# Performance work log

Hardware: AMD Instinct MI355X
Metric: run time of the kernel (lower is better)

Reference implementation:

```python
import math
import jax, jax.numpy as jnp
from jax import lax
import numpy as np

STRIDES = (4, 8, 16, 32, 64)
SIZES = (32, 64, 128, 256, 512)        # one anchor size per level
ASPECTS = (0.5, 1.0, 2.0)              # A = 3 anchors per location
GRIDS = ((336, 512), (168, 256), (84, 128), (42, 64), (21, 32))
OFFSET = 0.0
IMG_H, IMG_W = 1344, 2048
PRE_NMS_TOPK = 1000
POST_NMS_TOPK = 300
NMS_THRESH = 0.7
MIN_SIDE = 0.0
SCALE_CLAMP = math.log(1000.0 / 16.0)  # Box2BoxTransform default
NEG = -1e9                             # finite stand-in for removed/suppressed scores


def _cell_anchors(size):
    # AnchorGenerator.generate_cell_anchors
    area = float(size) ** 2
    out = []
    for ar in ASPECTS:
        w = math.sqrt(area / ar)
        h = ar * w
        out.append([-w / 2.0, -h / 2.0, w / 2.0, h / 2.0])
    return np.asarray(out, np.float32)  # [A,4]


def _level_anchors(level):
    # grid_anchors: shifts (x,y,x,y) + cell anchors, row-major over (y,x)
    gh, gw = GRIDS[level]
    s = float(STRIDES[level])
    sx = (np.arange(gw, dtype=np.float32) + OFFSET) * s
    sy = (np.arange(gh, dtype=np.float32) + OFFSET) * s
    yy, xx = np.meshgrid(sy, sx, indexing='ij')
    shifts = np.stack([xx.ravel(), yy.ravel(), xx.ravel(), yy.ravel()], axis=1)  # [H*W,4]
    cells = _cell_anchors(SIZES[level])  # [A,4]
    return jnp.asarray((shifts[:, None, :] + cells[None, :, :]).reshape(-1, 4))  # [H*W*A,4]


def _apply_deltas(deltas, anchors):
    # Box2BoxTransform.apply_deltas with unit weights. deltas/anchors: [N,K,4]
    w = anchors[..., 2] - anchors[..., 0]
    h = anchors[..., 3] - anchors[..., 1]
    cx = anchors[..., 0] + 0.5 * w
    cy = anchors[..., 1] + 0.5 * h
    dx, dy, dw, dh = (deltas[..., i] for i in range(4))
    pw = jnp.exp(jnp.minimum(dw, SCALE_CLAMP)) * w
    ph = jnp.exp(jnp.minimum(dh, SCALE_CLAMP)) * h
    pcx = dx * w + cx
    pcy = dy * h + cy
    return jnp.stack([pcx - 0.5 * pw, pcy - 0.5 * ph, pcx + 0.5 * pw, pcy + 0.5 * ph], axis=-1)


def _nms(boxes, scores, lvl):
    # batched NMS for one image: offset boxes per level so levels never suppress
    # each other, then iteratively pick argmax and suppress IoU > thresh.
    off = lvl * (float(max(IMG_H, IMG_W)) + 1.0)
    b = boxes + off[:, None]                               # [M,4]
    areas = (b[:, 2] - b[:, 0]) * (b[:, 3] - b[:, 1])

    def step(sc, _):
        i = jnp.argmax(sc)
        best = sc[i]
        lt = jnp.maximum(b[:, :2], b[i, :2])
        rb = jnp.minimum(b[:, 2:], b[i, 2:])
        wh = jnp.clip(rb - lt, 0.0)
        inter = wh[:, 0] * wh[:, 1]
        iou = inter / (areas + areas[i] - inter + 1e-9)
        sc = jnp.where(iou > NMS_THRESH, NEG, sc).at[i].set(NEG)
        return sc, (i, best > NEG * 0.5)

    _, (idx, valid) = lax.scan(step, scores, None, length=POST_NMS_TOPK)
    return idx, valid


def _forward(logits, deltas):
    # per-level sort (top-k) + gather, as in find_top_rpn_proposals
    all_scores, all_boxes, all_lvl = [], [], []
    for lv in range(5):
        sc, idx = lax.top_k(logits[lv], PRE_NMS_TOPK)                       # [N,K]
        d = jnp.take_along_axis(deltas[lv], idx[..., None], axis=1)          # [N,K,4]
        a = _level_anchors(lv)[idx]                                          # [N,K,4]
        all_boxes.append(_apply_deltas(d, a))
        all_scores.append(sc)
        all_lvl.append(jnp.full((PRE_NMS_TOPK,), float(lv), jnp.float32))
    scores = jnp.concatenate(all_scores, axis=1)   # [N, 5K]
    boxes = jnp.concatenate(all_boxes, axis=1)     # [N, 5K, 4]
    lvl = jnp.concatenate(all_lvl, axis=0)         # [5K]

    # _clip_box
    x0 = jnp.clip(boxes[..., 0], 0.0, float(IMG_W))
    y0 = jnp.clip(boxes[..., 1], 0.0, float(IMG_H))
    x1 = jnp.clip(boxes[..., 2], 0.0, float(IMG_W))
    y1 = jnp.clip(boxes[..., 3], 0.0, float(IMG_H))
    boxes = jnp.stack([x0, y0, x1, y1], axis=-1)

    # _nonempty_boxes: mask out instead of dynamic filter
    keep = ((x1 - x0) > MIN_SIDE) & ((y1 - y0) > MIN_SIDE)
    scores = jnp.where(keep, scores, NEG)

    idx, valid = jax.vmap(lambda b, s: _nms(b, s, lvl))(boxes, scores)       # [N,POST]
    ob = jnp.take_along_axis(boxes, idx[..., None], axis=1)                  # [N,POST,4]
    os = jnp.take_along_axis(scores, idx, axis=1)                            # [N,POST]
    ob = jnp.where(valid[..., None], ob, 0.0)
    os = jnp.where(valid, os, NEG)
    return jnp.concatenate([ob, os[..., None]], axis=-1)                     # [N,POST,5]


def setup_inputs() -> dict:
    key = jax.random.key(0)
    N = 8
    counts = [gh * gw * 3 for gh, gw in GRIDS]
    ks = jax.random.split(key, 10)
    inp = {}
    for lv, m in enumerate(counts):
        inp[f'logits{lv}'] = jax.random.normal(ks[2 * lv], (N, m), jnp.float32)
        inp[f'deltas{lv}'] = jax.random.normal(ks[2 * lv + 1], (N, m, 4), jnp.float32)
    return inp


def reference(logits0, deltas0, logits1, deltas1, logits2, deltas2,
              logits3, deltas3, logits4, deltas4):
    logits = [logits0, logits1, logits2, logits3, logits4]
    deltas = [deltas0, deltas1, deltas2, deltas3, deltas4]
    return _forward(logits, deltas)
```

## Files before the change

kernel.cpp:

```cpp
#include <hip/hip_runtime.h>
#include <cstdint>
#include <cstddef>

#define NB1      16384
#define L1SHIFT  18
#define K_TOP    1000
#define NCAND    5000
#define NIMG     8
#define NLVL     5
#define NTASK    40
#define NPOST    300
#define NEGF     (-1e9f)
#define NWORDS   79
#define NPAD     (NWORDS * 64)
#define NSLOT    23
#define SCAP     2048

typedef unsigned long long u64;

struct Ptrs {
    const float* lg[5];
    const float* dl[5];
};

__device__ __forceinline__ unsigned key_of(float f) {
    unsigned u = __float_as_uint(f);
    return (u & 0x80000000u) ? ~u : (u | 0x80000000u);
}

__device__ __forceinline__ void lvl_of_slot(int bx, int& lvl, int& lb, int& gx, int& m) {
    lvl = (bx < 16) ? 0 : (bx < 20) ? 1 : (bx < 21) ? 2 : (bx < 22) ? 3 : 4;
    const int S0[5] = {0, 16, 20, 21, 22};
    const int GX[5] = {16, 4, 1, 1, 1};
    const int MS[5] = {516096, 129024, 32256, 8064, 2016};
    lb = bx - S0[lvl];
    gx = GX[lvl];
    m  = MS[lvl];
}

__global__ __launch_bounds__(1024) void kStage(Ptrs p,
                                               u64* __restrict__ compS,
                                               unsigned* __restrict__ bcnt) {
    int lvl, lb, gx, m;
    lvl_of_slot(blockIdx.x, lvl, lb, gx, m);
    int img = blockIdx.y;
    size_t slice = (size_t)img * NSLOT + blockIdx.x;
    const float* lg = p.lg[lvl];
    const float TF5[5] = {2.75f, 2.3f, 1.7f, 0.9f, -0.35f};
    float Tf = TF5[lvl];
    __shared__ unsigned lcnt;
    int tid = threadIdx.x, lane = tid & 63;
    if (tid == 0) lcnt = 0u;
    __syncthreads();
    int m4 = m >> 2;
    int chunk4 = (m4 + gx - 1) / gx;
    int start4 = lb * chunk4;
    int end4   = min(start4 + chunk4, m4);
    const float4* src = (const float4*)(lg + (size_t)img * m);
    u64 below = (1ULL << lane) - 1ULL;
    for (int ib = start4; ib < end4; ib += 1024) {
        int i = ib + tid;
        bool inb = (i < end4);
        float4 v = inb ? src[i] : make_float4(0.f, 0.f, 0.f, 0.f);
        int j = i * 4;
        bool p0 = inb && (v.x > Tf);
        bool p1 = inb && (v.y > Tf);
        bool p2 = inb && (v.z > Tf);
        bool p3 = inb && (v.w > Tf);
        u64 m0 = __ballot(p0);
        u64 m1 = __ballot(p1);
        u64 m2 = __ballot(p2);
        u64 m3 = __ballot(p3);
        unsigned n0 = (unsigned)__popcll(m0), n1 = (unsigned)__popcll(m1);
        unsigned n2 = (unsigned)__popcll(m2), n3 = (unsigned)__popcll(m3);
        unsigned ntot = n0 + n1 + n2 + n3;
        unsigned base = 0;
        if (lane == 0 && ntot) base = atomicAdd(&lcnt, ntot);
        base = (unsigned)__shfl((int)base, 0, 64);
        if (p0) { unsigned q = base + (unsigned)__popcll(m0 & below);
                  if (q < SCAP) compS[slice * SCAP + q] = ((u64)key_of(v.x) << 32) | (unsigned)(~(unsigned)(j)); }
        if (p1) { unsigned q = base + n0 + (unsigned)__popcll(m1 & below);
                  if (q < SCAP) compS[slice * SCAP + q] = ((u64)key_of(v.y) << 32) | (unsigned)(~(unsigned)(j + 1)); }
        if (p2) { unsigned q = base + n0 + n1 + (unsigned)__popcll(m2 & below);
                  if (q < SCAP) compS[slice * SCAP + q] = ((u64)key_of(v.z) << 32) | (unsigned)(~(unsigned)(j + 2)); }
        if (p3) { unsigned q = base + n0 + n1 + n2 + (unsigned)__popcll(m3 & below);
                  if (q < SCAP) compS[slice * SCAP + q] = ((u64)key_of(v.w) << 32) | (unsigned)(~(unsigned)(j + 3)); }
    }
    __syncthreads();
    if (tid == 0) bcnt[slice] = lcnt;
}

__global__ __launch_bounds__(1024) void kSortSelect(
        Ptrs p,
        const u64* __restrict__ compS,
        const unsigned* __restrict__ bcnt,
        unsigned* __restrict__ histFB,
        float* __restrict__ cscore,
        float4* __restrict__ cbox,
        float4* __restrict__ cobox,
        unsigned* __restrict__ cog,
        unsigned* __restrict__ vcnt) {
    int task = blockIdx.x;
    int img = task / NLVL, lvl = task % NLVL;
    int tid = threadIdx.x, lane = tid & 63, wv = tid >> 6;
    const int   MS5[5]    = {516096, 129024, 32256, 8064, 2016};
    const int   GW[5]     = {512, 256, 128, 64, 32};
    const float STRIDEF[5]= {4.f, 8.f, 16.f, 32.f, 64.f};
    const int   SIZEI[5]  = {32, 64, 128, 256, 512};
    const float THI5[5]   = {2.97f, 2.5f, 1.95f, 1.25f, 0.15f};
    __shared__ u64 sure[1024];
    __shared__ u64 bnd[2048];
    __shared__ u64 su2[1024];
    __shared__ u64 bn2[1024];
    __shared__ unsigned sblkF[256];
    __shared__ int tmpF[8];
    __shared__ unsigned cS, cB;
    __shared__ unsigned soff[17];
    __shared__ int wTot[16];
    __shared__ int fbS;
    unsigned KH = key_of(THI5[lvl]);
    if (tid == 0) { cS = 0u; cB = 0u; }
    sure[tid] = 0ULL;
    bnd[tid] = 0ULL; bnd[tid + 1024] = 0ULL;
    if (tid < 17) soff[tid] = 0u;
    if (tid == 0) fbS = 0;
    __syncthreads();
    const int S0[5] = {0, 16, 20, 21, 22};
    const int NS[5] = {16, 4, 1, 1, 1};
    int s0 = S0[lvl], ns = NS[lvl];
    if (tid < ns) {
        unsigned raw = bcnt[(size_t)img * NSLOT + s0 + tid];
        if (raw > SCAP) atomicOr((unsigned*)&fbS, 1u);
        soff[tid + 1] = min(raw, (unsigned)SCAP);
    }
    __syncthreads();
    if (tid == 0)
        for (int s = 1; s <= 16; ++s) soff[s] += soff[s - 1];
    __syncthreads();
    int tot = (int)soff[ns];
    u64 below = (1ULL << lane) - 1ULL;
    for (int ib = 0; ib < tot; ib += 1024) {
        int idx = ib + tid;
        bool inb = (idx < tot);
        u64 c = 0ULL;
        if (inb) {
            int s = 0;
            while ((int)soff[s + 1] <= idx) ++s;
            c = compS[((size_t)img * NSLOT + s0 + s) * SCAP + (idx - (int)soff[s])];
        }
        bool pS = inb && ((unsigned)(c >> 32) > KH);
        bool pB = inb && !pS;
        u64 mS = __ballot(pS);
        u64 mB = __ballot(pB);
        unsigned bS = 0, bB = 0;
        if (lane == 0) {
            if (mS) bS = atomicAdd(&cS, (unsigned)__popcll(mS));
            if (mB) bB = atomicAdd(&cB, (unsigned)__popcll(mB));
        }
        bS = (unsigned)__shfl((int)bS, 0, 64);
        bB = (unsigned)__shfl((int)bB, 0, 64);
        if (pS) { unsigned q = bS + (unsigned)__popcll(mS & below); if (q < 1024u) sure[q] = c; }
        if (pB) { unsigned q = bB + (unsigned)__popcll(mB & below); if (q < 2048u) bnd[q] = c; }
    }
    __syncthreads();
    if (tid == 0) {
        if (cS > 1024u || cB > 2048u || (cS + cB) < (unsigned)K_TOP) fbS = 1;
    }
    __syncthreads();
    if (fbS) {
        int mm = MS5[lvl];
        int mm4 = mm >> 2;
        const float4* s4 = (const float4*)(p.lg[lvl] + (size_t)img * mm);
        unsigned* h = histFB + (size_t)task * NB1;
        for (int i = tid; i < NB1; i += 1024) h[i] = 0u;
        __syncthreads();
        for (int i = tid; i < mm4; i += 1024) {
            float4 v = s4[i];
            atomicAdd(&h[key_of(v.x) >> L1SHIFT], 1u);
            atomicAdd(&h[key_of(v.y) >> L1SHIFT], 1u);
            atomicAdd(&h[key_of(v.z) >> L1SHIFT], 1u);
            atomicAdd(&h[key_of(v.w) >> L1SHIFT], 1u);
        }
        __syncthreads();
        if (tid < 256) {
            unsigned coarse = 0;
            for (int ii = 0; ii < 64; ++ii) coarse += h[tid * 64 + ii];
            sblkF[tid] = coarse;
        }
        __syncthreads();
        unsigned SSv = 0;
        if (tid < 256) {
            SSv = sblkF[tid];
            for (int d = 1; d < 64; d <<= 1) {
                unsigned o = __shfl_down(SSv, d, 64);
                if (lane < 64 - d) SSv += o;
            }
            unsigned wtot = __shfl(SSv, 0, 64);
            if (lane == 0) tmpF[4 + wv] = (int)wtot;
        }
        __syncthreads();
        if (tid < 256) {
            unsigned add = 0;
            for (int w2 = wv + 1; w2 < 4; ++w2) add += (unsigned)tmpF[4 + w2];
            SSv += add;
            bool pred = (SSv >= (unsigned)K_TOP);
            u64 mk = __ballot(pred);
            if (lane == 0)
                tmpF[wv] = mk ? (wv * 64 + (63 - __builtin_clzll(mk))) : -1;
        }
        __syncthreads();
        int tb = max(max(tmpF[0], tmpF[1]), max(tmpF[2], tmpF[3]));
        __syncthreads();
        if (tid == 0) {
            unsigned above = 0;
            for (int b2 = tb + 1; b2 < 256; ++b2) above += sblkF[b2];
            unsigned rem = (unsigned)K_TOP - above;
            unsigned suf = 0;
            int pfx = tb * 64;
            for (int u2 = 63; u2 >= 0; --u2) {
                suf += h[tb * 64 + u2];
                if (suf >= rem) { pfx = tb * 64 + u2; break; }
            }
            tmpF[0] = pfx;
        }
        __syncthreads();
        unsigned pfx = (unsigned)tmpF[0];
        if (tid == 0) { cS = 0u; cB = 0u; }
        sure[tid] = 0ULL;
        bnd[tid] = 0ULL; bnd[tid + 1024] = 0ULL;
        __syncthreads();
        for (int ib = 0; ib < mm4; ib += 1024) {
            int i = ib + tid;
            bool inb = (i < mm4);
            float4 v = inb ? s4[i] : make_float4(0.f, 0.f, 0.f, 0.f);
            int j = i * 4;
            unsigned kk[4] = { key_of(v.x), key_of(v.y), key_of(v.z), key_of(v.w) };
#pragma unroll
            for (int e = 0; e < 4; ++e) {
                unsigned bin = kk[e] >> L1SHIFT;
                bool pS2 = inb && (bin > pfx);
                bool pB2 = inb && (bin == pfx);
                u64 mS2 = __ballot(pS2);
                u64 mB2 = __ballot(pB2);
                unsigned bS2 = 0, bB2 = 0;
                if (lane == 0) {
                    if (mS2) bS2 = atomicAdd(&cS, (unsigned)__popcll(mS2));
                    if (mB2) bB2 = atomicAdd(&cB, (unsigned)__popcll(mB2));
                }
                bS2 = (unsigned)__shfl((int)bS2, 0, 64);
                bB2 = (unsigned)__shfl((int)bB2, 0, 64);
                u64 cc = ((u64)kk[e] << 32) | (unsigned)(~(unsigned)(j + e));
                if (pS2) { unsigned q = bS2 + (unsigned)__popcll(mS2 & below); if (q < 1024u) sure[q] = cc; }
                if (pB2) { unsigned q = bB2 + (unsigned)__popcll(mB2 & below); if (q < 2048u) bnd[q] = cc; }
            }
        }
        __syncthreads();
    }
    unsigned S = cS;
    unsigned B = cB;
    u64 xs = sure[tid], xb = bnd[tid];
    int pp = 0;
    for (int k = 2; k <= 1024; k <<= 1) {
        for (int j = k >> 1; j > 0; j >>= 1) {
            bool up   = ((tid & k) == 0);
            bool iLow = ((tid & j) == 0);
            u64 ys, yb;
            if (j >= 64) {
                u64* sbuf = pp ? su2 : sure;
                u64* bbuf = pp ? bn2 : bnd;
                sbuf[tid] = xs; bbuf[tid] = xb;
                __syncthreads();
                ys = sbuf[tid ^ j]; yb = bbuf[tid ^ j];
                pp ^= 1;
            } else {
                ys = __shfl_xor(xs, j, 64);
                yb = __shfl_xor(xb, j, 64);
            }
            bool takeMax = (iLow == up);
            xs = takeMax ? ((xs > ys) ? xs : ys) : ((xs < ys) ? xs : ys);
            xb = takeMax ? ((xb > yb) ? xb : yb) : ((xb < yb) ? xb : yb);
        }
    }
    sure[tid] = xs; bnd[tid] = xb;
    __syncthreads();
    if (B > 1024) {
        for (int k = 2; k <= 2048; k <<= 1)
            for (int j = k >> 1; j > 0; j >>= 1) {
                int i = ((tid & ~(j - 1)) << 1) | (tid & (j - 1));
                int ppi = i | j;
                u64 A = bnd[i], Bv = bnd[ppi];
                bool up = ((i & k) == 0);
                if (up ? (A < Bv) : (A > Bv)) { bnd[i] = Bv; bnd[ppi] = A; }
                __syncthreads();
            }
    }
    int r = tid;
    u64 c = 0ULL;
    if (r < K_TOP) c = (r < (int)S) ? sure[r] : ((r - (int)S < (int)B) ? bnd[r - (int)S] : 0ULL);

    float sm = NEGF, x0 = 0.f, y0 = 0.f, x1 = 0.f, y1 = 0.f;
    float b0 = 0.f, b1 = 0.f, b2 = 0.f, b3 = 0.f;
    bool valid = false;
    if (r < K_TOP && c != 0ULL) {
        int idx = (int)(~(unsigned)c);
        int m = MS5[lvl];
        if ((unsigned)idx >= (unsigned)m) idx = 0;
        const float* lg = p.lg[lvl];
        const float* dl = p.dl[lvl];
        float score = lg[(size_t)img * m + idx];
        int a   = idx % 3;
        int loc = idx / 3;
        int gw  = GW[lvl];
        int x = loc % gw, y = loc / gw;
        double ssz = (double)SIZEI[lvl];
        double arr = (a == 0) ? 0.5 : ((a == 1) ? 1.0 : 2.0);
        double wd = sqrt(ssz * ssz / arr);
        double hd = arr * wd;
        float sx = (float)x * STRIDEF[lvl];
        float sy = (float)y * STRIDEF[lvl];
        float a0 = sx + (float)(-wd * 0.5);
        float a1 = sy + (float)(-hd * 0.5);
        float a2 = sx + (float)( wd * 0.5);
        float a3 = sy + (float)( hd * 0.5);
        float aw = a2 - a0, ah = a3 - a1;
        float acx = a0 + 0.5f * aw, acy = a1 + 0.5f * ah;
        size_t db = ((size_t)img * m + idx) * 4;
        float dx = dl[db], dy = dl[db + 1], dwv = dl[db + 2], dhv = dl[db + 3];
        const float CL = 4.135166556742356f;
        float pw = expf(fminf(dwv, CL)) * aw;
        float ph = expf(fminf(dhv, CL)) * ah;
        float pcx = dx * aw + acx;
        float pcy = dy * ah + acy;
        x0 = pcx - 0.5f * pw; y0 = pcy - 0.5f * ph;
        x1 = pcx + 0.5f * pw; y1 = pcy + 0.5f * ph;
        x0 = fminf(fmaxf(x0, 0.f), 2048.f);
        x1 = fminf(fmaxf(x1, 0.f), 2048.f);
        y0 = fminf(fmaxf(y0, 0.f), 1344.f);
        y1 = fminf(fmaxf(y1, 0.f), 1344.f);
        bool keep = ((x1 - x0) > 0.f) && ((y1 - y0) > 0.f);
        valid = keep;
        sm = score;
        float off = (float)lvl * 2049.0f;
        b0 = x0 + off; b1 = y0 + off; b2 = x1 + off; b3 = y1 + off;
    }
    u64 vm = __ballot(valid);
    int lanePre = (int)__popcll(vm & ((1ULL << lane) - 1ULL));
    if (lane == 0) wTot[wv] = (int)__popcll(vm);
    __syncthreads();
    int offset = 0, total = 0;
    for (int w2 = 0; w2 < 16; ++w2) {
        int t2 = wTot[w2];
        total += t2;
        if (w2 < wv) offset += t2;
    }
    int pos = offset + lanePre;
    if (valid) {
        int ci = img * NCAND + lvl * K_TOP + pos;
        cscore[ci] = sm;
        cbox[ci]   = make_float4(x0, y0, x1, y1);
        cobox[ci]  = make_float4(b0, b1, b2, b3);
        cog[ci]    = (unsigned)r;
    }
    if (tid == 0) vcnt[task] = (unsigned)total;
}

__global__ __launch_bounds__(1024) void kMergeRank(
        const float* __restrict__ cscore,
        const float4* __restrict__ cobox,
        const unsigned* __restrict__ cog,
        const unsigned* __restrict__ vcnt,
        float4* __restrict__ mobG,
        unsigned* __restrict__ midxG) {
    int task = blockIdx.x;
    int img = task / NLVL, lvl = task % NLVL;
    int tid = threadIdx.x;
    const int imgb = img * NCAND;
    __shared__ u64 compO[4 * K_TOP];
    __shared__ int LSs[NLVL];
    if (tid < NLVL) LSs[tid] = (int)vcnt[img * NLVL + tid];
    __syncthreads();
    for (int idx = tid; idx < 4 * K_TOP; idx += 1024) {
        int q = idx / K_TOP, gl2 = idx - q * K_TOP;
        int l2 = q + (q >= lvl ? 1 : 0);
        u64 c = 0ULL;
        if (gl2 < LSs[l2]) {
            int g2 = l2 * K_TOP + gl2;
            unsigned og = (unsigned)(l2 * K_TOP) + cog[imgb + g2];
            c = ((u64)key_of(cscore[imgb + g2]) << 32) | (unsigned)(~og);
        }
        compO[idx] = c;
    }
    __syncthreads();
    int gl = tid;
    if (gl < LSs[lvl]) {
        int g = lvl * K_TOP + gl;
        float4 pref = cobox[imgb + g];
        unsigned og = (unsigned)(lvl * K_TOP) + cog[imgb + g];
        u64 c = ((u64)key_of(cscore[imgb + g]) << 32) | (unsigned)(~og);
        int l0 = 0, h0 = LSs[0 + (0 >= lvl ? 1 : 0)];
        int l1 = 0, h1 = LSs[1 + (1 >= lvl ? 1 : 0)];
        int l2 = 0, h2 = LSs[2 + (2 >= lvl ? 1 : 0)];
        int l3 = 0, h3 = LSs[3 + (3 >= lvl ? 1 : 0)];
#pragma unroll
        for (int step = 0; step < 10; ++step) {
            if (l0 < h0) { int m0 = (l0 + h0) >> 1; if (compO[0 * K_TOP + m0] > c) l0 = m0 + 1; else h0 = m0; }
            if (l1 < h1) { int m1 = (l1 + h1) >> 1; if (compO[1 * K_TOP + m1] > c) l1 = m1 + 1; else h1 = m1; }
            if (l2 < h2) { int m2 = (l2 + h2) >> 1; if (compO[2 * K_TOP + m2] > c) l2 = m2 + 1; else h2 = m2; }
            if (l3 < h3) { int m3 = (l3 + h3) >> 1; if (compO[3 * K_TOP + m3] > c) l3 = m3 + 1; else h3 = m3; }
        }
        int pos = gl + l0 + l1 + l2 + l3;
        mobG[(size_t)img * NPAD + pos] = pref;
        midxG[imgb + pos] = (unsigned)g;
    }
}

__global__ __launch_bounds__(1024) void kScan(
        const float4* __restrict__ mobG,
        const unsigned* __restrict__ midxG,
        const float* __restrict__ cscore,
        const float4* __restrict__ cbox,
        const unsigned* __restrict__ vcnt,
        float* __restrict__ out) {
    int img = blockIdx.x;
    int tid = threadIdx.x;
    int lane = tid & 63;
    int wave = tid >> 6;
    __shared__ float4 wboxS[2][64];
    __shared__ u64    diagWS[64];
    __shared__ u64    partS[16];
    __shared__ float4 pboxAll[NPOST];
    __shared__ unsigned emS[NPOST];
    __shared__ int stateS[2];
    const int imgb = img * NCAND;

    int V = 0;
    for (int l = 0; l < NLVL; ++l) V += (int)vcnt[img * NLVL + l];

    if (tid < 64 && V > 0) wboxS[0][tid] = mobG[(size_t)img * NPAD + tid];
    __syncthreads();

    int emitted = 0;
    bool done = (V == 0);
    for (int w = 0; w < NWORDS && !done; ++w) {
        int base = w * 64;
        if (base >= V) break;
        int buf = w & 1;
        float4 bc = wboxS[buf][lane];
        float  arc = (bc.z - bc.x) * (bc.w - bc.y);
        bool supp = false;
        for (int t = wave; t < emitted; t += 16) {
            float4 bp = pboxAll[t];
            float arp = (bp.z - bp.x) * (bp.w - bp.y);
            float ltx = fmaxf(bc.x, bp.x), lty = fmaxf(bc.y, bp.y);
            float rbx = fminf(bc.z, bp.z), rby = fminf(bc.w, bp.w);
            float wx = fmaxf(rbx - ltx, 0.f), wy = fmaxf(rby - lty, 0.f);
            float inter = wx * wy;
            float denom = (arc + arp) - inter + 1e-9f;
            supp |= (inter / denom) > 0.7f;
        }
        u64 sb = __ballot(supp);
        if (lane == 0) partS[wave] = sb;
#pragma unroll
        for (int rr = 0; rr < 4; ++rr) {
            int r = wave * 4 + rr;
            float4 bp = wboxS[buf][r];
            float arp = (bp.z - bp.x) * (bp.w - bp.y);
            float ltx = fmaxf(bc.x, bp.x), lty = fmaxf(bc.y, bp.y);
            float rbx = fminf(bc.z, bp.z), rby = fminf(bc.w, bp.w);
            float wx = fmaxf(rbx - ltx, 0.f), wy = fmaxf(rby - lty, 0.f);
            float inter = wx * wy;
            float denom = (arc + arp) - inter + 1e-9f;
            bool pred = (inter / denom) > 0.7f;
            u64 db = __ballot(pred);
            if (lane == 0) diagWS[r] = db;
        }
        __syncthreads();
        if (wave == 0) {
            u64 dreg = diagWS[lane];
            u64 smv = partS[0];
#pragma unroll
            for (int q = 1; q < 16; ++q) smv |= partS[q];
            int rem = V - base;
            u64 vmask = (rem >= 64) ? ~0ULL : ((1ULL << rem) - 1ULL);
            u64 A = (~smv) & vmask;
            u64 below = (1ULL << lane) - 1ULL;
            bool inA = (A >> lane) & 1ULL;
            u64 S = A;
            while (true) {
                bool pred = inA && ((dreg & S & below) == 0ULL);
                u64 Snew = __ballot(pred);
                if (Snew == S) break;
                S = Snew;
            }
            int cnt = __popcll(S);
            int rem0 = NPOST - emitted;
            int rank = __popcll(S & below);
            bool kept = ((S >> lane) & 1ULL) && (rank < rem0);
            if (kept) {
                emS[emitted + rank]     = (unsigned)(base + lane);
                pboxAll[emitted + rank] = wboxS[buf][lane];
            }
            if (lane == 0) {
                int emadd = (cnt < rem0) ? cnt : rem0;
                stateS[0] = emitted + emadd;
                stateS[1] = (cnt >= rem0) ? 1 : 0;
            }
        } else if (wave == 15) {
            int nb = base + 64;
            if (nb < V && (w + 1) < NWORDS)
                wboxS[buf ^ 1][lane] = mobG[(size_t)img * NPAD + nb + lane];
        }
        __syncthreads();
        emitted = stateS[0];
        done = (stateS[1] != 0);
    }
    __syncthreads();
    for (int rr = tid; rr < NPOST; rr += 1024) {
        float* o = out + ((size_t)img * NPOST + rr) * 5;
        if (rr < emitted) {
            unsigned i = emS[rr];
            unsigned g = midxG[imgb + i];
            float4 cb = cbox[imgb + g];
            float sc = cscore[imgb + g];
            o[0] = cb.x; o[1] = cb.y; o[2] = cb.z; o[3] = cb.w; o[4] = sc;
        } else {
            o[0] = 0.f; o[1] = 0.f; o[2] = 0.f; o[3] = 0.f; o[4] = NEGF;
        }
    }
}

extern "C" void kernel_launch(void* const* d_in, const int* in_sizes, int n_in,
                              void* d_out, int out_size, void* d_ws, size_t ws_size,
                              hipStream_t stream) {
    Ptrs P;
    for (int l = 0; l < 5; ++l) {
        P.lg[l] = (const float*)d_in[2 * l];
        P.dl[l] = (const float*)d_in[2 * l + 1];
    }
    char* w = (char*)d_ws;
    size_t off = 0;
    auto alloc = [&](size_t bytes) -> void* {
        void* pp = (void*)(w + off);
        off = (off + bytes + 255) & ~(size_t)255;
        return pp;
    };
    unsigned* bcnt   = (unsigned*)alloc((size_t)NIMG * NSLOT * 4);
    u64* compS       = (u64*)alloc((size_t)NIMG * NSLOT * SCAP * 8);
    unsigned* histFB = (unsigned*)alloc((size_t)NTASK * NB1 * 4);
    float*  cscore   = (float*)alloc((size_t)NTASK * K_TOP * 4);
    float4* cbox     = (float4*)alloc((size_t)NTASK * K_TOP * 16);
    float4* cobox    = (float4*)alloc((size_t)NTASK * K_TOP * 16);
    unsigned* cog    = (unsigned*)alloc((size_t)NTASK * K_TOP * 4);
    unsigned* vcnt   = (unsigned*)alloc(NTASK * 4);
    float4* mobG     = (float4*)alloc((size_t)NIMG * NPAD * 16);
    unsigned* midxG  = (unsigned*)alloc((size_t)NIMG * NCAND * 4);
    (void)in_sizes; (void)n_in; (void)out_size; (void)ws_size;

    kStage<<<dim3(NSLOT, NIMG), 1024, 0, stream>>>(P, compS, bcnt);
    kSortSelect<<<NTASK, 1024, 0, stream>>>(P, compS, bcnt, histFB,
                                            cscore, cbox, cobox, cog, vcnt);
    kMergeRank<<<NTASK, 1024, 0, stream>>>(cscore, cobox, cog, vcnt, mobG, midxG);
    kScan<<<NIMG, 1024, 0, stream>>>(mobG, midxG, cscore, cbox, vcnt,
                                     (float*)d_out);
}
```

Measured before the change: 61.55 us.

## Fuse merge-rank into NMS scan kernel, keeping sorted order in shared memory

The separate merge-rank kernel, which ran 40 blocks, is folded into the per-image scan kernel. Each image block now builds all 5000 sort keys in shared memory, computes merged positions by binary search, and keeps the sorted index permutation in LDS. This removes one kernel launch and the global round trip through mobG/midxG. In exchange, the ranking work moves onto only 8 blocks, so each block does five times as much, and the larger shared-memory footprint may lower occupancy.

```diff
diff --git a/kernel.cpp b/kernel.cpp
--- a/kernel.cpp
+++ b/kernel.cpp
@@ -12,7 +12,6 @@
 #define NPOST    300
 #define NEGF     (-1e9f)
 #define NWORDS   79
-#define NPAD     (NWORDS * 64)
 #define NSLOT    23
 #define SCAP     2048
 
@@ -364,67 +363,20 @@
     if (tid == 0) vcnt[task] = (unsigned)total;
 }
 
-__global__ __launch_bounds__(1024) void kMergeRank(
+__global__ __launch_bounds__(1024) void kMergeScan(
         const float* __restrict__ cscore,
+        const float4* __restrict__ cbox,
         const float4* __restrict__ cobox,
         const unsigned* __restrict__ cog,
-        const unsigned* __restrict__ vcnt,
-        float4* __restrict__ mobG,
-        unsigned* __restrict__ midxG) {
-    int task = blockIdx.x;
-    int img = task / NLVL, lvl = task % NLVL;
-    int tid = threadIdx.x;
-    const int imgb = img * NCAND;
-    __shared__ u64 compO[4 * K_TOP];
-    __shared__ int LSs[NLVL];
-    if (tid < NLVL) LSs[tid] = (int)vcnt[img * NLVL + tid];
-    __syncthreads();
-    for (int idx = tid; idx < 4 * K_TOP; idx += 1024) {
-        int q = idx / K_TOP, gl2 = idx - q * K_TOP;
-        int l2 = q + (q >= lvl ? 1 : 0);
-        u64 c = 0ULL;
-        if (gl2 < LSs[l2]) {
-            int g2 = l2 * K_TOP + gl2;
-            unsigned og = (unsigned)(l2 * K_TOP) + cog[imgb + g2];
-            c = ((u64)key_of(cscore[imgb + g2]) << 32) | (unsigned)(~og);
-        }
-        compO[idx] = c;
-    }
-    __syncthreads();
-    int gl = tid;
-    if (gl < LSs[lvl]) {
-        int g = lvl * K_TOP + gl;
-        float4 pref = cobox[imgb + g];
-        unsigned og = (unsigned)(lvl * K_TOP) + cog[imgb + g];
-        u64 c = ((u64)key_of(cscore[imgb + g]) << 32) | (unsigned)(~og);
-        int l0 = 0, h0 = LSs[0 + (0 >= lvl ? 1 : 0)];
-        int l1 = 0, h1 = LSs[1 + (1 >= lvl ? 1 : 0)];
-        int l2 = 0, h2 = LSs[2 + (2 >= lvl ? 1 : 0)];
-        int l3 = 0, h3 = LSs[3 + (3 >= lvl ? 1 : 0)];
-#pragma unroll
-        for (int step = 0; step < 10; ++step) {
-            if (l0 < h0) { int m0 = (l0 + h0) >> 1; if (compO[0 * K_TOP + m0] > c) l0 = m0 + 1; else h0 = m0; }
-            if (l1 < h1) { int m1 = (l1 + h1) >> 1; if (compO[1 * K_TOP + m1] > c) l1 = m1 + 1; else h1 = m1; }
-            if (l2 < h2) { int m2 = (l2 + h2) >> 1; if (compO[2 * K_TOP + m2] > c) l2 = m2 + 1; else h2 = m2; }
-            if (l3 < h3) { int m3 = (l3 + h3) >> 1; if (compO[3 * K_TOP + m3] > c) l3 = m3 + 1; else h3 = m3; }
-        }
-        int pos = gl + l0 + l1 + l2 + l3;
-        mobG[(size_t)img * NPAD + pos] = pref;
-        midxG[imgb + pos] = (unsigned)g;
-    }
-}
-
-__global__ __launch_bounds__(1024) void kScan(
-        const float4* __restrict__ mobG,
-        const unsigned* __restrict__ midxG,
-        const float* __restrict__ cscore,
-        const float4* __restrict__ cbox,
         const unsigned* __restrict__ vcnt,
         float* __restrict__ out) {
     int img = blockIdx.x;
     int tid = threadIdx.x;
     int lane = tid & 63;
     int wave = tid >> 6;
+    __shared__ u64 compA[NCAND];
+    __shared__ unsigned sIdx[NCAND];
+    __shared__ int LSs[NLVL];
     __shared__ float4 wboxS[2][64];
     __shared__ u64    diagWS[64];
     __shared__ u64    partS[16];
@@ -433,10 +385,47 @@
     __shared__ int stateS[2];
     const int imgb = img * NCAND;
 
-    int V = 0;
-    for (int l = 0; l < NLVL; ++l) V += (int)vcnt[img * NLVL + l];
-
-    if (tid < 64 && V > 0) wboxS[0][tid] = mobG[(size_t)img * NPAD + tid];
+    if (tid < NLVL) LSs[tid] = (int)vcnt[img * NLVL + tid];
+    __syncthreads();
+    int V = LSs[0] + LSs[1] + LSs[2] + LSs[3] + LSs[4];
+
+    for (int idx = tid; idx < NCAND; idx += 1024) {
+        int l = idx / K_TOP, gl = idx - l * K_TOP;
+        u64 c = 0ULL;
+        if (gl < LSs[l]) {
+            unsigned og = (unsigned)(l * K_TOP) + cog[imgb + idx];
+            c = ((u64)key_of(cscore[imgb + idx]) << 32) | (unsigned)(~og);
+        }
+        compA[idx] = c;
+    }
+    __syncthreads();
+    for (int idx = tid; idx < NCAND; idx += 1024) {
+        int l = idx / K_TOP, gl = idx - l * K_TOP;
+        if (gl >= LSs[l]) continue;
+        u64 c = compA[idx];
+        int o0 = 0 + (0 >= l ? 1 : 0);
+        int o1 = 1 + (1 >= l ? 1 : 0);
+        int o2 = 2 + (2 >= l ? 1 : 0);
+        int o3 = 3 + (3 >= l ? 1 : 0);
+        int l0 = 0, h0 = LSs[o0];
+        int l1 = 0, h1 = LSs[o1];
+        int l2 = 0, h2 = LSs[o2];
+        int l3 = 0, h3 = LSs[o3];
+#pragma unroll
+        for (int step = 0; step < 10; ++step) {
+            if (l0 < h0) { int m0 = (l0 + h0) >> 1; if (compA[o0 * K_TOP + m0] > c) l0 = m0 + 1; else h0 = m0; }
+            if (l1 < h1) { int m1 = (l1 + h1) >> 1; if (compA[o1 * K_TOP + m1] > c) l1 = m1 + 1; else h1 = m1; }
+            if (l2 < h2) { int m2 = (l2 + h2) >> 1; if (compA[o2 * K_TOP + m2] > c) l2 = m2 + 1; else h2 = m2; }
+            if (l3 < h3) { int m3 = (l3 + h3) >> 1; if (compA[o3 * K_TOP + m3] > c) l3 = m3 + 1; else h3 = m3; }
+        }
+        int pos = gl + l0 + l1 + l2 + l3;
+        sIdx[pos] = (unsigned)idx;
+    }
+    __syncthreads();
+
+    if (tid < 64)
+        wboxS[0][tid] = (tid < V) ? cobox[imgb + (int)sIdx[tid]]
+                                  : make_float4(0.f, 0.f, 0.f, 0.f);
     __syncthreads();
 
     int emitted = 0;
@@ -507,8 +496,11 @@
             }
         } else if (wave == 15) {
             int nb = base + 64;
-            if (nb < V && (w + 1) < NWORDS)
-                wboxS[buf ^ 1][lane] = mobG[(size_t)img * NPAD + nb + lane];
+            if (nb < V && (w + 1) < NWORDS) {
+                int src = nb + lane;
+                wboxS[buf ^ 1][lane] = (src < V) ? cobox[imgb + (int)sIdx[src]]
+                                                 : make_float4(0.f, 0.f, 0.f, 0.f);
+            }
         }
         __syncthreads();
         emitted = stateS[0];
@@ -518,8 +510,7 @@
     for (int rr = tid; rr < NPOST; rr += 1024) {
         float* o = out + ((size_t)img * NPOST + rr) * 5;
         if (rr < emitted) {
-            unsigned i = emS[rr];
-            unsigned g = midxG[imgb + i];
+            unsigned g = sIdx[emS[rr]];
             float4 cb = cbox[imgb + g];
             float sc = cscore[imgb + g];
             o[0] = cb.x; o[1] = cb.y; o[2] = cb.z; o[3] = cb.w; o[4] = sc;
@@ -552,14 +543,11 @@
     float4* cobox    = (float4*)alloc((size_t)NTASK * K_TOP * 16);
     unsigned* cog    = (unsigned*)alloc((size_t)NTASK * K_TOP * 4);
     unsigned* vcnt   = (unsigned*)alloc(NTASK * 4);
-    float4* mobG     = (float4*)alloc((size_t)NIMG * NPAD * 16);
-    unsigned* midxG  = (unsigned*)alloc((size_t)NIMG * NCAND * 4);
     (void)in_sizes; (void)n_in; (void)out_size; (void)ws_size;
 
     kStage<<<dim3(NSLOT, NIMG), 1024, 0, stream>>>(P, compS, bcnt);
     kSortSelect<<<NTASK, 1024, 0, stream>>>(P, compS, bcnt, histFB,
                                             cscore, cbox, cobox, cog, vcnt);
-    kMergeRank<<<NTASK, 1024, 0, stream>>>(cscore, cobox, cog, vcnt, mobG, midxG);
-    kScan<<<NIMG, 1024, 0, stream>>>(mobG, midxG, cscore, cbox, vcnt,
-                                     (float*)d_out);
+    kMergeScan<<<NIMG, 1024, 0, stream>>>(cscore, cbox, cobox, cog, vcnt,
+                                          (float*)d_out);
 }
```

After: 68.70 us. 1.12x slower.
